# Kernel tuning notes

Measured on AMD Instinct MI355X. Metric: run time of the kernel, lower is better.

The kernel has to match this reference:

```python
import jax, jax.numpy as jnp
import numpy as np

V, E, H, L = 32000, 512, 1024, 2
B, S, T = 32, 64, 64


def setup_inputs() -> dict:
    key = jax.random.key(0)
    ks = jax.random.split(key, 16)
    sd = 0.05
    p = lambda k, shape: (jax.random.normal(k, shape, jnp.float32) * sd)
    z = lambda shape: jnp.zeros(shape, jnp.float32)
    return {
        "tgt_batch": jax.random.randint(ks[0], (B, S), 0, V),
        "enc_h": p(ks[1], (L, B, H)),
        "enc_c": p(ks[2], (L, B, H)),
        "enc_outputs": p(ks[3], (T, B, H)),
        "emb": p(ks[4], (V, E)),
        "W_ih0": p(ks[5], (4 * H, E + H)),
        "W_hh0": p(ks[6], (4 * H, H)),
        "b_ih0": z((4 * H,)),
        "b_hh0": z((4 * H,)),
        "W_ih1": p(ks[7], (4 * H, H)),
        "W_hh1": p(ks[8], (4 * H, H)),
        "b_ih1": z((4 * H,)),
        "b_hh1": z((4 * H,)),
        "Wa": p(ks[9], (H, 2 * H)),
        "ba": z((H,)),
        "va": p(ks[10], (H,)),
        "Wc": p(ks[11], (H, 2 * H)),
        "bc": z((H,)),
        "Wo": p(ks[12], (V, H)),
        "bo": z((V,)),
        "teacher_forcing": 1,
    }


def _lstm_cell(x, h, c, Wih, Whh, bih, bhh):
    # PyTorch gate order: i, f, g, o
    g = x @ Wih.T + bih + h @ Whh.T + bhh
    i, f, gg, o = jnp.split(g, 4, axis=1)
    c2 = jax.nn.sigmoid(f) * c + jax.nn.sigmoid(i) * jnp.tanh(gg)
    return jax.nn.sigmoid(o) * jnp.tanh(c2), c2


def reference(tgt_batch, enc_h, enc_c, enc_outputs, emb,
              W_ih0, W_hh0, b_ih0, b_hh0, W_ih1, W_hh1, b_ih1, b_hh1,
              Wa, ba, va, Wc, bc, Wo, bo, teacher_forcing):
    # teacher_forcing == 1 -> always feed the gold previous word (matches
    # the torch loop, whose sampling branch is never taken at tf=1.0).
    tgt = tgt_batch.T  # [S, B], seq-first

    def step(carry, x_t):
        h, c, attn_h = carry  # h,c: [L,B,H]; attn_h: [B,H]
        x = jnp.concatenate([emb[x_t], attn_h], axis=1)  # [B, E+H]
        h0, c0 = _lstm_cell(x, h[0], c[0], W_ih0, W_hh0, b_ih0, b_hh0)
        h1, c1 = _lstm_cell(h0, h[1], c[1], W_ih1, W_hh1, b_ih1, b_hh1)
        # additive ('concat') attention over encoder states, query = top h
        hid = jnp.broadcast_to(h1[None], enc_outputs.shape)  # [T,B,H]
        energy = jnp.tanh(jnp.concatenate([hid, enc_outputs], axis=-1) @ Wa.T + ba)
        scores = jnp.einsum('tbh,h->bt', energy, va)  # [B,T]
        weights = jax.nn.softmax(scores, axis=1)
        context = jnp.einsum('bt,tbh->bh', weights, enc_outputs)  # [B,H]
        attn_h2 = jnp.tanh(jnp.concatenate([h1, context], axis=1) @ Wc.T + bc)
        logp = jax.nn.log_softmax(attn_h2 @ Wo.T + bo, axis=1)  # [B,V]
        return (jnp.stack([h0, h1]), jnp.stack([c0, c1]), attn_h2), logp

    init = (enc_h, enc_c, jnp.zeros((tgt.shape[1], H), enc_h.dtype))
    _, dec_outputs = jax.lax.scan(step, init, tgt[:-1])  # [S-1, B, V]
    dec_output_words = jnp.argmax(dec_outputs, axis=-1).astype(jnp.int32)
    return dec_outputs, dec_output_words
```

## Files before the change

### kernel.cpp

```cpp
#include <hip/hip_runtime.h>
#include <math.h>

#define VOCAB 32000
#define EMBD  512
#define HID   1024
#define BATCH 32
#define SEQ   64
#define TENC  64
#define NSTEP 63
#define G4    4096

typedef __attribute__((ext_vector_type(8))) short short8;
typedef __attribute__((ext_vector_type(4))) float f32x4;
typedef __attribute__((ext_vector_type(4))) unsigned short us4;
typedef unsigned short u16;

__device__ __forceinline__ float4 ld4(const float* p) {
  return *reinterpret_cast<const float4*>(p);
}
__device__ __forceinline__ u16 f2bf(float x) {
  unsigned u = __float_as_uint(x);
  return (u16)((u + 0x7fffu + ((u >> 16) & 1u)) >> 16);
}
__device__ __forceinline__ float bf2f(u16 h) {
  return __uint_as_float(((unsigned)h) << 16);
}

template<int MODE>
__device__ __forceinline__ void mfma32(
    const u16* __restrict__ Xahi, const u16* __restrict__ Xalo,
    const u16* __restrict__ Xbhi, const u16* __restrict__ Xblo,
    const u16* __restrict__ Whi,  const u16* __restrict__ Wlo,
    int nt, float* res)
{
  const int tid = threadIdx.x;
  const int w = tid >> 6, l = tid & 63;
  const int c = l & 15, koct = l >> 4;
  constexpr int K   = (MODE == 0) ? 2048 : 1024;
  constexpr int WS  = (MODE == 0) ? 2048 : 1024;
  constexpr int SPW = K / 32 / 4;
  const int r0 = c, r1 = 16 + c;
  const int wr0 = (MODE == 0) ? ((r0 >> 3)*1024 + nt*8 + (r0 & 7)) : (nt*32 + r0);
  const int wr1 = (MODE == 0) ? ((r1 >> 3)*1024 + nt*8 + (r1 & 7)) : (nt*32 + r1);
  const u16* bh0 = Whi + (size_t)wr0 * WS;
  const u16* bh1 = Whi + (size_t)wr1 * WS;
  const u16* bl0 = Wlo + (size_t)wr0 * WS;
  const u16* bl1 = Wlo + (size_t)wr1 * WS;

  auto ldA = [&](int m, int kg, int lo) -> short8 {
    const u16* base;
    if (MODE == 0 && kg >= 1024) base = lo ? Xblo : Xbhi;
    else                         base = lo ? Xalo : Xahi;
    const int b = m*16 + c;
    return *reinterpret_cast<const short8*>(base + b*1024 + (kg & 1023));
  };

  f32x4 acc[2][2];
  #pragma unroll
  for (int m = 0; m < 2; ++m)
    #pragma unroll
    for (int n = 0; n < 2; ++n) acc[m][n] = (f32x4){0.f,0.f,0.f,0.f};

  const int s0 = w * SPW;
  short8 Ah[2], Al[2], Bh[2], Bl[2];
  {
    const int kg = s0*32 + koct*8;
    Ah[0]=ldA(0,kg,0); Ah[1]=ldA(1,kg,0); Al[0]=ldA(0,kg,1); Al[1]=ldA(1,kg,1);
    Bh[0]=*reinterpret_cast<const short8*>(bh0+kg);
    Bh[1]=*reinterpret_cast<const short8*>(bh1+kg);
    Bl[0]=*reinterpret_cast<const short8*>(bl0+kg);
    Bl[1]=*reinterpret_cast<const short8*>(bl1+kg);
  }
  for (int s = s0; s < s0 + SPW; ++s) {
    short8 nAh[2], nAl[2], nBh[2], nBl[2];
    if (s + 1 < s0 + SPW) {
      const int kg = (s+1)*32 + koct*8;
      nAh[0]=ldA(0,kg,0); nAh[1]=ldA(1,kg,0); nAl[0]=ldA(0,kg,1); nAl[1]=ldA(1,kg,1);
      nBh[0]=*reinterpret_cast<const short8*>(bh0+kg);
      nBh[1]=*reinterpret_cast<const short8*>(bh1+kg);
      nBl[0]=*reinterpret_cast<const short8*>(bl0+kg);
      nBl[1]=*reinterpret_cast<const short8*>(bl1+kg);
    }
    #pragma unroll
    for (int n = 0; n < 2; ++n)
      #pragma unroll
      for (int m = 0; m < 2; ++m) {
        acc[m][n] = __builtin_amdgcn_mfma_f32_16x16x32_bf16(Ah[m], Bh[n], acc[m][n], 0, 0, 0);
        acc[m][n] = __builtin_amdgcn_mfma_f32_16x16x32_bf16(Ah[m], Bl[n], acc[m][n], 0, 0, 0);
        acc[m][n] = __builtin_amdgcn_mfma_f32_16x16x32_bf16(Al[m], Bh[n], acc[m][n], 0, 0, 0);
      }
    #pragma unroll
    for (int i = 0; i < 2; ++i) { Ah[i]=nAh[i]; Al[i]=nAl[i]; Bh[i]=nBh[i]; Bl[i]=nBl[i]; }
  }
  #pragma unroll
  for (int m = 0; m < 2; ++m)
    #pragma unroll
    for (int n = 0; n < 2; ++n)
      #pragma unroll
      for (int r = 0; r < 4; ++r) {
        const int b = m*16 + koct*4 + r;
        const int rr = n*16 + c;
        res[w*1056 + b*33 + rr] = acc[m][n][r];
      }
}

struct GKM {
  const u16 *Xahi, *Xalo, *Xbhi, *Xblo;
  const u16 *Whi, *Wlo;
  const float* bsum; const float* gembt;
  float* c; u16 *hhi; u16 *hlo;
};

template<int HASGEMB>
__global__ __launch_bounds__(256) void gates_mfma_k(GKM P) {
  __shared__ float res[4*1056];
  mfma32<0>(P.Xahi, P.Xalo, P.Xbhi, P.Xblo, P.Whi, P.Wlo, blockIdx.x, res);
  __syncthreads();
  const int tid = threadIdx.x;
  const int b = tid >> 3, j = tid & 7;
  const int n = blockIdx.x*8 + j;
  float g4[4];
  #pragma unroll
  for (int g = 0; g < 4; ++g) {
    const int r = g*8 + j;
    float s = P.bsum[g*1024 + n]
            + res[b*33+r] + res[1056 + b*33+r] + res[2112 + b*33+r] + res[3168 + b*33+r];
    if (HASGEMB) s += P.gembt[(size_t)b*G4 + g*1024 + n];
    g4[g] = s;
  }
  const float si = 1.f/(1.f+expf(-g4[0]));
  const float sf = 1.f/(1.f+expf(-g4[1]));
  const float so = 1.f/(1.f+expf(-g4[3]));
  const int i = b*HID + n;
  const float cn = sf*P.c[i] + si*tanhf(g4[2]);
  P.c[i] = cn;
  const float h = so*tanhf(cn);
  const u16 hh = f2bf(h);
  P.hhi[i] = hh;
  P.hlo[i] = f2bf(h - bf2f(hh));
}

struct PKM {
  const u16 *Xhi, *Xlo; const u16 *Whi, *Wlo; float* Pq;
};

__global__ __launch_bounds__(256) void proj_mfma_k(PKM P) {
  __shared__ float res[4*1056];
  mfma32<1>(P.Xhi, P.Xlo, nullptr, nullptr, P.Whi, P.Wlo, blockIdx.x, res);
  __syncthreads();
  const int tid = threadIdx.x;
  #pragma unroll
  for (int q = 0; q < 4; ++q) {
    const int o = q*256 + tid;
    const int b = o >> 5, r = o & 31;
    const float s = res[b*33+r] + res[1056 + b*33+r]
                  + res[2112 + b*33+r] + res[3168 + b*33+r];
    P.Pq[(size_t)b*2048 + blockIdx.x*32 + r] = s;
  }
}

struct AKM {
  const float* Pq; const float* PreAC; const float* va; const float* bc;
  u16* AHthi; u16* AHtlo;
};

__global__ __launch_bounds__(1024) void attn_k(AKM P) {
  __shared__ float QS[HID];
  __shared__ float sw[TENC];
  __shared__ float W64[TENC];
  const int b = blockIdx.x;
  const int tid = threadIdx.x;
  QS[tid] = P.Pq[(size_t)b*2048 + tid];
  __syncthreads();
  const int lane = tid & 63, wid = tid >> 6;
  float vreg[16];
  #pragma unroll
  for (int i2 = 0; i2 < 16; ++i2) vreg[i2] = P.va[lane + 64*i2];
  #pragma unroll
  for (int j = 0; j < 4; ++j) {
    const int te = wid*4 + j;
    const float* pr = P.PreAC + ((size_t)te*BATCH + b)*2048;
    float s = 0.f;
    #pragma unroll
    for (int i2 = 0; i2 < 16; ++i2) {
      const int idx = lane + 64*i2;
      s += vreg[i2] * tanhf(QS[idx] + pr[idx]);
    }
    #pragma unroll
    for (int off = 32; off; off >>= 1) s += __shfl_xor(s, off);
    if (lane == 0) sw[te] = s;
  }
  __syncthreads();
  if (tid < TENC) {
    const float v = sw[tid];
    float mx = v;
    #pragma unroll
    for (int off = 32; off; off >>= 1) mx = fmaxf(mx, __shfl_xor(mx, off));
    const float e = expf(v - mx);
    float sum = e;
    #pragma unroll
    for (int off = 32; off; off >>= 1) sum += __shfl_xor(sum, off);
    W64[tid] = e / sum;
  }
  __syncthreads();
  const int hh = tid;
  float acc = 0.f;
  #pragma unroll 8
  for (int te = 0; te < TENC; ++te)
    acc += W64[te] * P.PreAC[((size_t)te*BATCH + b)*2048 + HID + hh];
  const float hc = P.Pq[(size_t)b*2048 + HID + hh] + P.bc[hh];
  const float ah = tanhf(acc + hc);
  const u16 ahh = f2bf(ah);
  P.AHthi[(size_t)b*HID + hh] = ahh;
  P.AHtlo[(size_t)b*HID + hh] = f2bf(ah - bf2f(ahh));
}

template<int MODE>
__global__ __launch_bounds__(256) void pack_k(const float* __restrict__ A,
                                              const float* __restrict__ B,
                                              u16* __restrict__ hi, u16* __restrict__ lo) {
  constexpr int ROWS = (MODE == 2) ? 2048 : 4096;
  constexpr int K    = (MODE == 2) ? 1024 : 2048;
  const size_t total = (size_t)ROWS * (K/4);
  for (size_t i = (size_t)blockIdx.x*256 + threadIdx.x; i < total;
       i += (size_t)gridDim.x*256) {
    const int row = (int)(i / (K/4));
    const int k = (int)(i % (K/4)) * 4;
    float4 v;
    if (MODE == 0) v = (k < 1024) ? ld4(A + (size_t)row*1536 + 512 + k)
                                  : ld4(B + (size_t)row*1024 + (k - 1024));
    else if (MODE == 1) v = (k < 1024) ? ld4(A + (size_t)row*1024 + k)
                                       : ld4(B + (size_t)row*1024 + (k - 1024));
    else v = (row < 1024) ? ld4(A + (size_t)row*2048 + k)
                          : ld4(B + (size_t)(row - 1024)*2048 + k);
    us4 h, l;
    h.x = f2bf(v.x); l.x = f2bf(v.x - bf2f(h.x));
    h.y = f2bf(v.y); l.y = f2bf(v.y - bf2f(h.y));
    h.z = f2bf(v.z); l.z = f2bf(v.z - bf2f(h.z));
    h.w = f2bf(v.w); l.w = f2bf(v.w - bf2f(h.w));
    *reinterpret_cast<us4*>(hi + i*4) = h;
    *reinterpret_cast<us4*>(lo + i*4) = l;
  }
}

__global__ __launch_bounds__(256) void cvt_k(const float* __restrict__ src,
                                             u16* __restrict__ hi,
                                             u16* __restrict__ lo, int n) {
  int i = (blockIdx.x*256 + threadIdx.x) * 4;
  const int stride = gridDim.x * 256 * 4;
  for (; i < n; i += stride) {
    const float4 v = ld4(src + i);
    us4 h, l;
    h.x = f2bf(v.x); l.x = f2bf(v.x - bf2f(h.x));
    h.y = f2bf(v.y); l.y = f2bf(v.y - bf2f(h.y));
    h.z = f2bf(v.z); l.z = f2bf(v.z - bf2f(h.z));
    h.w = f2bf(v.w); l.w = f2bf(v.w - bf2f(h.w));
    *reinterpret_cast<us4*>(hi + i) = h;
    *reinterpret_cast<us4*>(lo + i) = l;
  }
}

struct WGP {
  const float* A; const float* W; const float* W2; const float* bias;
  const int* tgt; const float* emb;
  float* C; int ldc;
};

template<int WM>
__device__ __forceinline__ float4 ldWL(const WGP& P, int r, int k) {
  if (WM == 2) return ld4(P.W + (size_t)r * (EMBD + HID) + k);
  if (r < HID) return ld4(P.W  + (size_t)r * (2*HID) + HID + k);
  return ld4(P.W2 + (size_t)(r - HID) * (2*HID) + HID + k);
}

template<int WM>
__device__ __forceinline__ float4 ldAL(const WGP& P, int row, int k) {
  if (WM == 2) {
    const int tok = P.tgt[(row & 31) * SEQ + (row >> 5)];
    return ld4(P.emb + (size_t)tok * EMBD + k);
  }
  return ld4(P.A + (size_t)row * 1024 + k);
}

template<int WM>
__global__ __launch_bounds__(256, 2) void gemmL(WGP P) {
  constexpr int KK = (WM == 2) ? 512 : 1024;
  __shared__ float At[32*36];
  __shared__ float Wt[32*260];
  const int tid = threadIdx.x;
  const int m0 = blockIdx.x * 32;
  const int n0 = blockIdx.y * 256;
  const int lr = tid >> 3, lc = (tid & 7) << 2;
  const int tn = tid & 31, tm = tid >> 5;
  float acc[4][8];
  #pragma unroll
  for (int i = 0; i < 4; ++i)
    #pragma unroll
    for (int x = 0; x < 8; ++x) acc[i][x] = 0.f;

  float4 av = ldAL<WM>(P, m0 + lr, lc);
  float4 wv[8];
  #pragma unroll
  for (int it = 0; it < 8; ++it) wv[it] = ldWL<WM>(P, n0 + lr + it*32, lc);

  for (int k0 = 0; k0 < KK; k0 += 32) {
    float4 avn, wvn[8];
    if (k0 + 32 < KK) {
      avn = ldAL<WM>(P, m0 + lr, k0 + 32 + lc);
      #pragma unroll
      for (int it = 0; it < 8; ++it) wvn[it] = ldWL<WM>(P, n0 + lr + it*32, k0 + 32 + lc);
    }
    __syncthreads();
    At[(lc+0)*36+lr]=av.x; At[(lc+1)*36+lr]=av.y; At[(lc+2)*36+lr]=av.z; At[(lc+3)*36+lr]=av.w;
    #pragma unroll
    for (int it = 0; it < 8; ++it) {
      const int r = lr + it*32;
      Wt[(lc+0)*260+r]=wv[it].x; Wt[(lc+1)*260+r]=wv[it].y;
      Wt[(lc+2)*260+r]=wv[it].z; Wt[(lc+3)*260+r]=wv[it].w;
    }
    __syncthreads();
    #pragma unroll
    for (int kk = 0; kk < 32; ++kk) {
      const float4 a  = *reinterpret_cast<const float4*>(&At[kk*36 + tm*4]);
      const float4 w0 = *reinterpret_cast<const float4*>(&Wt[kk*260 + tn*8]);
      const float4 w1 = *reinterpret_cast<const float4*>(&Wt[kk*260 + tn*8 + 4]);
      #pragma unroll
      for (int i = 0; i < 4; ++i) {
        const float ai = (&a.x)[i];
        acc[i][0]+=ai*w0.x; acc[i][1]+=ai*w0.y; acc[i][2]+=ai*w0.z; acc[i][3]+=ai*w0.w;
        acc[i][4]+=ai*w1.x; acc[i][5]+=ai*w1.y; acc[i][6]+=ai*w1.z; acc[i][7]+=ai*w1.w;
      }
    }
    av = avn;
    #pragma unroll
    for (int it = 0; it < 8; ++it) wv[it] = wvn[it];
  }
  const int na = n0 + tn*8, ma = m0 + tm*4;
  float bb[8];
  #pragma unroll
  for (int x = 0; x < 8; ++x) {
    if (WM == 1) bb[x] = (na + x < HID) ? P.bias[na+x] : 0.f;
    else         bb[x] = 0.f;
  }
  #pragma unroll
  for (int i = 0; i < 4; ++i)
    #pragma unroll
    for (int x = 0; x < 8; ++x)
      P.C[(size_t)(ma+i)*P.ldc + na + x] = acc[i][x] + bb[x];
}

struct LM {
  const u16* Ahi; const u16* Alo;
  const u16* Bhi; const u16* Blo;
  const float* bo; float* out;
};

__global__ __launch_bounds__(256) void logits_mfma(LM P) {
  __shared__ u16 sA[2][4][64][8];
  __shared__ u16 sB[2][4][128][8];
  const int tid = threadIdx.x;
  const int m0 = blockIdx.x * 64;
  const int n0 = blockIdx.y * 128;
  const int w = tid >> 6, l = tid & 63;
  const int mb = (w & 1) * 32, nb = (w >> 1) * 64;
  f32x4 acc[2][4];
  #pragma unroll
  for (int mt = 0; mt < 2; ++mt)
    #pragma unroll
    for (int nt = 0; nt < 4; ++nt) acc[mt][nt] = (f32x4){0.f,0.f,0.f,0.f};

  const int arow = tid >> 2, akg = tid & 3;
  const int brow = tid >> 1, bkg = (tid & 1) * 2;
  short8 pah, pal, pbh0, pbh1, pbl0, pbl1;
  {
    const size_t ao = (size_t)(m0 + arow)*HID + akg*8;
    const size_t bo0 = (size_t)(n0 + brow)*HID + bkg*8;
    pah  = *reinterpret_cast<const short8*>(P.Ahi + ao);
    pal  = *reinterpret_cast<const short8*>(P.Alo + ao);
    pbh0 = *reinterpret_cast<const short8*>(P.Bhi + bo0);
    pbh1 = *reinterpret_cast<const short8*>(P.Bhi + bo0 + 8);
    pbl0 = *reinterpret_cast<const short8*>(P.Blo + bo0);
    pbl1 = *reinterpret_cast<const short8*>(P.Blo + bo0 + 8);
  }
  for (int kc = 0; kc < 32; ++kc) {
    __syncthreads();
    *reinterpret_cast<short8*>(&sA[0][akg][arow][0]) = pah;
    *reinterpret_cast<short8*>(&sA[1][akg][arow][0]) = pal;
    *reinterpret_cast<short8*>(&sB[0][bkg  ][brow][0]) = pbh0;
    *reinterpret_cast<short8*>(&sB[0][bkg+1][brow][0]) = pbh1;
    *reinterpret_cast<short8*>(&sB[1][bkg  ][brow][0]) = pbl0;
    *reinterpret_cast<short8*>(&sB[1][bkg+1][brow][0]) = pbl1;
    __syncthreads();
    if (kc + 1 < 32) {
      const size_t ao = (size_t)(m0 + arow)*HID + (kc+1)*32 + akg*8;
      const size_t bo0 = (size_t)(n0 + brow)*HID + (kc+1)*32 + bkg*8;
      pah  = *reinterpret_cast<const short8*>(P.Ahi + ao);
      pal  = *reinterpret_cast<const short8*>(P.Alo + ao);
      pbh0 = *reinterpret_cast<const short8*>(P.Bhi + bo0);
      pbh1 = *reinterpret_cast<const short8*>(P.Bhi + bo0 + 8);
      pbl0 = *reinterpret_cast<const short8*>(P.Blo + bo0);
      pbl1 = *reinterpret_cast<const short8*>(P.Blo + bo0 + 8);
    }
    const int kg = l >> 4, rr = l & 15;
    short8 ah[2], al[2];
    #pragma unroll
    for (int mt = 0; mt < 2; ++mt) {
      ah[mt] = *reinterpret_cast<const short8*>(&sA[0][kg][mb + mt*16 + rr][0]);
      al[mt] = *reinterpret_cast<const short8*>(&sA[1][kg][mb + mt*16 + rr][0]);
    }
    #pragma unroll
    for (int nt = 0; nt < 4; ++nt) {
      const short8 bh = *reinterpret_cast<const short8*>(&sB[0][kg][nb + nt*16 + rr][0]);
      const short8 bl = *reinterpret_cast<const short8*>(&sB[1][kg][nb + nt*16 + rr][0]);
      #pragma unroll
      for (int mt = 0; mt < 2; ++mt) {
        acc[mt][nt] = __builtin_amdgcn_mfma_f32_16x16x32_bf16(ah[mt], bh, acc[mt][nt], 0, 0, 0);
        acc[mt][nt] = __builtin_amdgcn_mfma_f32_16x16x32_bf16(ah[mt], bl, acc[mt][nt], 0, 0, 0);
        acc[mt][nt] = __builtin_amdgcn_mfma_f32_16x16x32_bf16(al[mt], bh, acc[mt][nt], 0, 0, 0);
      }
    }
  }
  #pragma unroll
  for (int mt = 0; mt < 2; ++mt) {
    #pragma unroll
    for (int nt = 0; nt < 4; ++nt) {
      #pragma unroll
      for (int r = 0; r < 4; ++r) {
        const int row = m0 + mb + mt*16 + (l >> 4)*4 + r;
        const int col = n0 + nb + nt*16 + (l & 15);
        if (row < NSTEP*BATCH)
          P.out[(size_t)row*VOCAB + col] = acc[mt][nt][r] + P.bo[col];
      }
    }
  }
}

__global__ __launch_bounds__(256) void lsm_k(float* __restrict__ out,
                                             float* __restrict__ words) {
  const int b = blockIdx.x;
  const int t = blockIdx.y;
  float* row = out + ((size_t)t*BATCH + b)*VOCAB;
  const int tid = threadIdx.x;
  float m = -INFINITY; int mi = 0;
  for (int v = tid; v < VOCAB; v += 256) {
    const float x = row[v];
    if (x > m) { m = x; mi = v; }
  }
  __shared__ float sm[256]; __shared__ int si[256];
  sm[tid] = m; si[tid] = mi;
  __syncthreads();
  for (int s2 = 128; s2; s2 >>= 1) {
    if (tid < s2) {
      const float om = sm[tid+s2]; const int oi = si[tid+s2];
      if (om > sm[tid] || (om == sm[tid] && oi < si[tid])) { sm[tid]=om; si[tid]=oi; }
    }
    __syncthreads();
  }
  const float mx = sm[0]; const int amax = si[0];
  float s = 0.f;
  for (int v = tid; v < VOCAB; v += 256) s += expf(row[v]-mx);
  __shared__ float ss[256];
  ss[tid] = s; __syncthreads();
  for (int s2=128; s2; s2>>=1) { if (tid < s2) ss[tid] += ss[tid+s2]; __syncthreads(); }
  const float lse = logf(ss[0]) + mx;
  for (int v = tid; v < VOCAB; v += 256) row[v] = row[v] - lse;
  if (tid == 0) words[(size_t)t*BATCH + b] = (float)amax;
}

__global__ __launch_bounds__(256) void init_k(const float* __restrict__ enc_h,
                                              const float* __restrict__ enc_c,
                                              const float* __restrict__ bih0,
                                              const float* __restrict__ bhh0,
                                              const float* __restrict__ bih1,
                                              const float* __restrict__ bhh1,
                                              float* c0, float* c1,
                                              u16* h0hi, u16* h0lo, u16* h1hi, u16* h1lo,
                                              u16* zahhi, u16* zahlo,
                                              float* bsum0, float* bsum1) {
  const int i = blockIdx.x*256 + threadIdx.x;
  if (i < BATCH*HID) {
    c0[i] = enc_c[i]; c1[i] = enc_c[BATCH*HID + i];
    const float v0 = enc_h[i];
    const u16 h0 = f2bf(v0);
    h0hi[i] = h0; h0lo[i] = f2bf(v0 - bf2f(h0));
    const float v1 = enc_h[BATCH*HID + i];
    const u16 h1 = f2bf(v1);
    h1hi[i] = h1; h1lo[i] = f2bf(v1 - bf2f(h1));
    zahhi[i] = 0; zahlo[i] = 0;
  }
  if (i < G4) {
    bsum0[i] = bih0[i] + bhh0[i];
    bsum1[i] = bih1[i] + bhh1[i];
  }
}

extern "C" void kernel_launch(void* const* d_in, const int* in_sizes, int n_in,
                              void* d_out, int out_size, void* d_ws, size_t ws_size,
                              hipStream_t stream) {
  const int*   tgt   = (const int*)d_in[0];
  const float* enc_h = (const float*)d_in[1];
  const float* enc_c = (const float*)d_in[2];
  const float* enc   = (const float*)d_in[3];
  const float* emb   = (const float*)d_in[4];
  const float* Wih0  = (const float*)d_in[5];
  const float* Whh0  = (const float*)d_in[6];
  const float* bih0  = (const float*)d_in[7];
  const float* bhh0  = (const float*)d_in[8];
  const float* Wih1  = (const float*)d_in[9];
  const float* Whh1  = (const float*)d_in[10];
  const float* bih1  = (const float*)d_in[11];
  const float* bhh1  = (const float*)d_in[12];
  const float* Wa    = (const float*)d_in[13];
  const float* ba    = (const float*)d_in[14];
  const float* va    = (const float*)d_in[15];
  const float* Wc    = (const float*)d_in[16];
  const float* bc    = (const float*)d_in[17];
  const float* Wo    = (const float*)d_in[18];
  const float* bo    = (const float*)d_in[19];

  u16* AHhi = (u16*)d_ws;
  u16* AHlo = AHhi + (size_t)2048*1024;
  float* pool = (float*)(AHlo + (size_t)2048*1024);

  float* PreAC = pool;
  float* Gemb  = PreAC + (size_t)2048*2048;
  float* Pq    = Gemb  + (size_t)NSTEP*BATCH*G4;
  float* c0    = Pq    + (size_t)BATCH*2048;
  float* c1v   = c0    + BATCH*HID;
  float* bsum0 = c1v   + BATCH*HID;
  float* bsum1 = bsum0 + G4;
  u16* W0hi = (u16*)(bsum1 + G4);
  u16* W0lo = W0hi + (size_t)4096*2048;
  u16* W1hi = W0lo + (size_t)4096*2048;
  u16* W1lo = W1hi + (size_t)4096*2048;
  u16* WAhi = W1lo + (size_t)4096*2048;
  u16* WAlo = WAhi + (size_t)2048*1024;
  u16* h0Ahi = WAlo + (size_t)2048*1024;
  u16* h0Alo = h0Ahi + BATCH*HID;
  u16* h0Bhi = h0Alo + BATCH*HID;
  u16* h0Blo = h0Bhi + BATCH*HID;
  u16* h1Ahi = h0Blo + BATCH*HID;
  u16* h1Alo = h1Ahi + BATCH*HID;
  u16* h1Bhi = h1Alo + BATCH*HID;
  u16* h1Blo = h1Bhi + BATCH*HID;
  u16* zahhi = h1Blo + BATCH*HID;
  u16* zahlo = zahhi + BATCH*HID;
  u16* Wohi = (u16*)pool;
  u16* Wolo = Wohi + (size_t)VOCAB*1024;

  float* out   = (float*)d_out;
  float* words = out + (size_t)NSTEP*BATCH*VOCAB;

  init_k<<<dim3(128), 256, 0, stream>>>(enc_h, enc_c, bih0, bhh0, bih1, bhh1,
                                        c0, c1v, h0Ahi, h0Alo, h1Ahi, h1Alo,
                                        zahhi, zahlo, bsum0, bsum1);

  {
    WGP p = {}; p.A = enc; p.W = Wa; p.W2 = Wc; p.bias = ba; p.C = PreAC; p.ldc = 2048;
    gemmL<1><<<dim3(64, 8), 256, 0, stream>>>(p);
  }
  {
    WGP p = {}; p.W = Wih0; p.tgt = tgt; p.emb = emb; p.C = Gemb; p.ldc = G4;
    gemmL<2><<<dim3(NSTEP*BATCH/32, G4/256), 256, 0, stream>>>(p);
  }
  pack_k<0><<<dim3(1024), 256, 0, stream>>>(Wih0, Whh0, W0hi, W0lo);
  pack_k<1><<<dim3(1024), 256, 0, stream>>>(Wih1, Whh1, W1hi, W1lo);
  pack_k<2><<<dim3(512), 256, 0, stream>>>(Wa, Wc, WAhi, WAlo);

  for (int t = 0; t < NSTEP; ++t) {
    const u16* ahphi = t ? (AHhi + (size_t)(t-1)*BATCH*HID) : zahhi;
    const u16* ahplo = t ? (AHlo + (size_t)(t-1)*BATCH*HID) : zahlo;
    const u16* h0phi = (t & 1) ? h0Bhi : h0Ahi;
    const u16* h0plo = (t & 1) ? h0Blo : h0Alo;
    u16* h0chi = (t & 1) ? h0Ahi : h0Bhi;
    u16* h0clo = (t & 1) ? h0Alo : h0Blo;
    const u16* h1phi = (t & 1) ? h1Bhi : h1Ahi;
    const u16* h1plo = (t & 1) ? h1Blo : h1Alo;
    u16* h1chi = (t & 1) ? h1Ahi : h1Bhi;
    u16* h1clo = (t & 1) ? h1Alo : h1Blo;

    {
      GKM p = {};
      p.Xahi = ahphi; p.Xalo = ahplo; p.Xbhi = h0phi; p.Xblo = h0plo;
      p.Whi = W0hi; p.Wlo = W0lo;
      p.bsum = bsum0; p.gembt = Gemb + (size_t)t*BATCH*G4;
      p.c = c0; p.hhi = h0chi; p.hlo = h0clo;
      gates_mfma_k<1><<<dim3(128), 256, 0, stream>>>(p);
    }
    {
      GKM p = {};
      p.Xahi = h0chi; p.Xalo = h0clo; p.Xbhi = h1phi; p.Xblo = h1plo;
      p.Whi = W1hi; p.Wlo = W1lo;
      p.bsum = bsum1; p.gembt = nullptr;
      p.c = c1v; p.hhi = h1chi; p.hlo = h1clo;
      gates_mfma_k<0><<<dim3(128), 256, 0, stream>>>(p);
    }
    {
      PKM p; p.Xhi = h1chi; p.Xlo = h1clo; p.Whi = WAhi; p.Wlo = WAlo; p.Pq = Pq;
      proj_mfma_k<<<dim3(64), 256, 0, stream>>>(p);
    }
    {
      AKM p; p.Pq = Pq; p.PreAC = PreAC; p.va = va; p.bc = bc;
      p.AHthi = AHhi + (size_t)t*BATCH*HID;
      p.AHtlo = AHlo + (size_t)t*BATCH*HID;
      attn_k<<<dim3(BATCH), 1024, 0, stream>>>(p);
    }
  }

  cvt_k<<<dim3(4096), 256, 0, stream>>>(Wo, Wohi, Wolo, VOCAB*1024);
  {
    LM p; p.Ahi = AHhi; p.Alo = AHlo; p.Bhi = Wohi; p.Blo = Wolo;
    p.bo = bo; p.out = out;
    logits_mfma<<<dim3(32, VOCAB/128), 256, 0, stream>>>(p);
  }
  lsm_k<<<dim3(BATCH, NSTEP), 256, 0, stream>>>(out, words);
}
```

Baseline: 5.914 ms.

## Move encoder and embedding precompute GEMMs to split-bf16 MFMA tile kernel

Adds a generic split-bf16 MFMA tile kernel, with an optional token-gather on the A operand, and uses it for the encoder attention projection and the embedding input-gate precompute. These previously ran through the older gemmL path. Inputs are first converted to hi/lo bf16 pairs in extra workspace, with a fallback to the old path when the workspace is too small. The logits GEMM now uses the same kernel with a 1D grid. Log-softmax switches to an online max/sum in one pass with 512 threads.

New measurement: 6.062 ms. +2.5%, slower.

```diff
diff --git a/kernel.cpp b/kernel.cpp
--- a/kernel.cpp
+++ b/kernel.cpp
@@ -215,12 +215,114 @@
   P.AHtlo[(size_t)b*HID + hh] = f2bf(ah - bf2f(ahh));
 }
 
+struct TM {
+  const u16 *Ahi, *Alo, *Bhi, *Blo;
+  const int* tgt; const float* bias;
+  float* out; int ldc, M, ntile_n;
+};
+
+template<int NC, int AMODE>
+__global__ __launch_bounds__(256) void tile_k(TM P) {
+  __shared__ float smemf[6144];
+  u16* sA = (u16*)smemf;
+  u16* sB = sA + 4096;
+  constexpr int K = NC * 32;
+  const int tile = blockIdx.x;
+  const int mi = tile / P.ntile_n, ni = tile % P.ntile_n;
+  const int m0 = mi * 64, n0 = ni * 128;
+  const int tid = threadIdx.x;
+  const int w = tid >> 6, l = tid & 63;
+  const int mb = (w & 1) * 32, nb = (w >> 1) * 64;
+  f32x4 acc[2][4];
+  #pragma unroll
+  for (int mt = 0; mt < 2; ++mt)
+    #pragma unroll
+    for (int nt = 0; nt < 4; ++nt) acc[mt][nt] = (f32x4){0.f,0.f,0.f,0.f};
+
+  const int arow = tid >> 2, akg = tid & 3;
+  const int brow = tid >> 1, bkg = (tid & 1) * 2;
+  size_t arbase;
+  if (AMODE == 1) {
+    const int row = m0 + arow;
+    const int tok = P.tgt[(row & 31)*SEQ + (row >> 5)];
+    arbase = (size_t)tok * K;
+  } else {
+    arbase = (size_t)(m0 + arow) * K;
+  }
+  const size_t brbase = (size_t)(n0 + brow) * K;
+
+  short8 pah, pal, pbh0, pbh1, pbl0, pbl1;
+  {
+    const size_t ao = arbase + akg*8;
+    const size_t bo0 = brbase + bkg*8;
+    pah  = *reinterpret_cast<const short8*>(P.Ahi + ao);
+    pal  = *reinterpret_cast<const short8*>(P.Alo + ao);
+    pbh0 = *reinterpret_cast<const short8*>(P.Bhi + bo0);
+    pbh1 = *reinterpret_cast<const short8*>(P.Bhi + bo0 + 8);
+    pbl0 = *reinterpret_cast<const short8*>(P.Blo + bo0);
+    pbl1 = *reinterpret_cast<const short8*>(P.Blo + bo0 + 8);
+  }
+  for (int kc = 0; kc < NC; ++kc) {
+    __syncthreads();
+    *reinterpret_cast<short8*>(sA + ((0*4 + akg)*64 + arow)*8) = pah;
+    *reinterpret_cast<short8*>(sA + ((1*4 + akg)*64 + arow)*8) = pal;
+    *reinterpret_cast<short8*>(sB + ((0*4 + bkg  )*128 + brow)*8) = pbh0;
+    *reinterpret_cast<short8*>(sB + ((0*4 + bkg+1)*128 + brow)*8) = pbh1;
+    *reinterpret_cast<short8*>(sB + ((1*4 + bkg  )*128 + brow)*8) = pbl0;
+    *reinterpret_cast<short8*>(sB + ((1*4 + bkg+1)*128 + brow)*8) = pbl1;
+    __syncthreads();
+    if (kc + 1 < NC) {
+      const size_t ao = arbase + (kc+1)*32 + akg*8;
+      const size_t bo0 = brbase + (kc+1)*32 + bkg*8;
+      pah  = *reinterpret_cast<const short8*>(P.Ahi + ao);
+      pal  = *reinterpret_cast<const short8*>(P.Alo + ao);
+      pbh0 = *reinterpret_cast<const short8*>(P.Bhi + bo0);
+      pbh1 = *reinterpret_cast<const short8*>(P.Bhi + bo0 + 8);
+      pbl0 = *reinterpret_cast<const short8*>(P.Blo + bo0);
+      pbl1 = *reinterpret_cast<const short8*>(P.Blo + bo0 + 8);
+    }
+    const int kg = l >> 4, rr = l & 15;
+    short8 ah[2], al[2];
+    #pragma unroll
+    for (int mt = 0; mt < 2; ++mt) {
+      ah[mt] = *reinterpret_cast<const short8*>(sA + ((0*4 + kg)*64 + mb + mt*16 + rr)*8);
+      al[mt] = *reinterpret_cast<const short8*>(sA + ((1*4 + kg)*64 + mb + mt*16 + rr)*8);
+    }
+    #pragma unroll
+    for (int nt = 0; nt < 4; ++nt) {
+      const short8 bh = *reinterpret_cast<const short8*>(sB + ((0*4 + kg)*128 + nb + nt*16 + rr)*8);
+      const short8 bl = *reinterpret_cast<const short8*>(sB + ((1*4 + kg)*128 + nb + nt*16 + rr)*8);
+      #pragma unroll
+      for (int mt = 0; mt < 2; ++mt) {
+        acc[mt][nt] = __builtin_amdgcn_mfma_f32_16x16x32_bf16(ah[mt], bh, acc[mt][nt], 0, 0, 0);
+        acc[mt][nt] = __builtin_amdgcn_mfma_f32_16x16x32_bf16(ah[mt], bl, acc[mt][nt], 0, 0, 0);
+        acc[mt][nt] = __builtin_amdgcn_mfma_f32_16x16x32_bf16(al[mt], bh, acc[mt][nt], 0, 0, 0);
+      }
+    }
+  }
+  #pragma unroll
+  for (int mt = 0; mt < 2; ++mt) {
+    #pragma unroll
+    for (int nt = 0; nt < 4; ++nt) {
+      #pragma unroll
+      for (int r = 0; r < 4; ++r) {
+        const int row = m0 + mb + mt*16 + (l >> 4)*4 + r;
+        const int col = n0 + nb + nt*16 + (l & 15);
+        if (row < P.M) {
+          const float bb = P.bias ? P.bias[col] : 0.f;
+          P.out[(size_t)row*P.ldc + col] = acc[mt][nt][r] + bb;
+        }
+      }
+    }
+  }
+}
+
 template<int MODE>
 __global__ __launch_bounds__(256) void pack_k(const float* __restrict__ A,
                                               const float* __restrict__ B,
                                               u16* __restrict__ hi, u16* __restrict__ lo) {
-  constexpr int ROWS = (MODE == 2) ? 2048 : 4096;
-  constexpr int K    = (MODE == 2) ? 1024 : 2048;
+  constexpr int ROWS = (MODE == 2 || MODE == 3) ? 2048 : 4096;
+  constexpr int K    = (MODE == 2 || MODE == 3) ? 1024 : (MODE == 4 ? 512 : 2048);
   const size_t total = (size_t)ROWS * (K/4);
   for (size_t i = (size_t)blockIdx.x*256 + threadIdx.x; i < total;
        i += (size_t)gridDim.x*256) {
@@ -231,8 +333,11 @@
                                   : ld4(B + (size_t)row*1024 + (k - 1024));
     else if (MODE == 1) v = (k < 1024) ? ld4(A + (size_t)row*1024 + k)
                                        : ld4(B + (size_t)row*1024 + (k - 1024));
-    else v = (row < 1024) ? ld4(A + (size_t)row*2048 + k)
-                          : ld4(B + (size_t)(row - 1024)*2048 + k);
+    else if (MODE == 2) v = (row < 1024) ? ld4(A + (size_t)row*2048 + k)
+                                         : ld4(B + (size_t)(row - 1024)*2048 + k);
+    else if (MODE == 3) v = (row < 1024) ? ld4(A + (size_t)row*2048 + 1024 + k)
+                                         : ld4(B + (size_t)(row - 1024)*2048 + 1024 + k);
+    else v = ld4(A + (size_t)row*1536 + k);
     us4 h, l;
     h.x = f2bf(v.x); l.x = f2bf(v.x - bf2f(h.x));
     h.y = f2bf(v.y); l.y = f2bf(v.y - bf2f(h.y));
@@ -349,121 +454,39 @@
       P.C[(size_t)(ma+i)*P.ldc + na + x] = acc[i][x] + bb[x];
 }
 
-struct LM {
-  const u16* Ahi; const u16* Alo;
-  const u16* Bhi; const u16* Blo;
-  const float* bo; float* out;
-};
-
-__global__ __launch_bounds__(256) void logits_mfma(LM P) {
-  __shared__ u16 sA[2][4][64][8];
-  __shared__ u16 sB[2][4][128][8];
-  const int tid = threadIdx.x;
-  const int m0 = blockIdx.x * 64;
-  const int n0 = blockIdx.y * 128;
-  const int w = tid >> 6, l = tid & 63;
-  const int mb = (w & 1) * 32, nb = (w >> 1) * 64;
-  f32x4 acc[2][4];
-  #pragma unroll
-  for (int mt = 0; mt < 2; ++mt)
-    #pragma unroll
-    for (int nt = 0; nt < 4; ++nt) acc[mt][nt] = (f32x4){0.f,0.f,0.f,0.f};
-
-  const int arow = tid >> 2, akg = tid & 3;
-  const int brow = tid >> 1, bkg = (tid & 1) * 2;
-  short8 pah, pal, pbh0, pbh1, pbl0, pbl1;
-  {
-    const size_t ao = (size_t)(m0 + arow)*HID + akg*8;
-    const size_t bo0 = (size_t)(n0 + brow)*HID + bkg*8;
-    pah  = *reinterpret_cast<const short8*>(P.Ahi + ao);
-    pal  = *reinterpret_cast<const short8*>(P.Alo + ao);
-    pbh0 = *reinterpret_cast<const short8*>(P.Bhi + bo0);
-    pbh1 = *reinterpret_cast<const short8*>(P.Bhi + bo0 + 8);
-    pbl0 = *reinterpret_cast<const short8*>(P.Blo + bo0);
-    pbl1 = *reinterpret_cast<const short8*>(P.Blo + bo0 + 8);
-  }
-  for (int kc = 0; kc < 32; ++kc) {
-    __syncthreads();
-    *reinterpret_cast<short8*>(&sA[0][akg][arow][0]) = pah;
-    *reinterpret_cast<short8*>(&sA[1][akg][arow][0]) = pal;
-    *reinterpret_cast<short8*>(&sB[0][bkg  ][brow][0]) = pbh0;
-    *reinterpret_cast<short8*>(&sB[0][bkg+1][brow][0]) = pbh1;
-    *reinterpret_cast<short8*>(&sB[1][bkg  ][brow][0]) = pbl0;
-    *reinterpret_cast<short8*>(&sB[1][bkg+1][brow][0]) = pbl1;
-    __syncthreads();
-    if (kc + 1 < 32) {
-      const size_t ao = (size_t)(m0 + arow)*HID + (kc+1)*32 + akg*8;
-      const size_t bo0 = (size_t)(n0 + brow)*HID + (kc+1)*32 + bkg*8;
-      pah  = *reinterpret_cast<const short8*>(P.Ahi + ao);
-      pal  = *reinterpret_cast<const short8*>(P.Alo + ao);
-      pbh0 = *reinterpret_cast<const short8*>(P.Bhi + bo0);
-      pbh1 = *reinterpret_cast<const short8*>(P.Bhi + bo0 + 8);
-      pbl0 = *reinterpret_cast<const short8*>(P.Blo + bo0);
-      pbl1 = *reinterpret_cast<const short8*>(P.Blo + bo0 + 8);
-    }
-    const int kg = l >> 4, rr = l & 15;
-    short8 ah[2], al[2];
-    #pragma unroll
-    for (int mt = 0; mt < 2; ++mt) {
-      ah[mt] = *reinterpret_cast<const short8*>(&sA[0][kg][mb + mt*16 + rr][0]);
-      al[mt] = *reinterpret_cast<const short8*>(&sA[1][kg][mb + mt*16 + rr][0]);
-    }
-    #pragma unroll
-    for (int nt = 0; nt < 4; ++nt) {
-      const short8 bh = *reinterpret_cast<const short8*>(&sB[0][kg][nb + nt*16 + rr][0]);
-      const short8 bl = *reinterpret_cast<const short8*>(&sB[1][kg][nb + nt*16 + rr][0]);
-      #pragma unroll
-      for (int mt = 0; mt < 2; ++mt) {
-        acc[mt][nt] = __builtin_amdgcn_mfma_f32_16x16x32_bf16(ah[mt], bh, acc[mt][nt], 0, 0, 0);
-        acc[mt][nt] = __builtin_amdgcn_mfma_f32_16x16x32_bf16(ah[mt], bl, acc[mt][nt], 0, 0, 0);
-        acc[mt][nt] = __builtin_amdgcn_mfma_f32_16x16x32_bf16(al[mt], bh, acc[mt][nt], 0, 0, 0);
-      }
-    }
-  }
-  #pragma unroll
-  for (int mt = 0; mt < 2; ++mt) {
-    #pragma unroll
-    for (int nt = 0; nt < 4; ++nt) {
-      #pragma unroll
-      for (int r = 0; r < 4; ++r) {
-        const int row = m0 + mb + mt*16 + (l >> 4)*4 + r;
-        const int col = n0 + nb + nt*16 + (l & 15);
-        if (row < NSTEP*BATCH)
-          P.out[(size_t)row*VOCAB + col] = acc[mt][nt][r] + P.bo[col];
-      }
-    }
-  }
-}
-
-__global__ __launch_bounds__(256) void lsm_k(float* __restrict__ out,
+__global__ __launch_bounds__(512) void lsm_k(float* __restrict__ out,
                                              float* __restrict__ words) {
   const int b = blockIdx.x;
   const int t = blockIdx.y;
   float* row = out + ((size_t)t*BATCH + b)*VOCAB;
   const int tid = threadIdx.x;
-  float m = -INFINITY; int mi = 0;
-  for (int v = tid; v < VOCAB; v += 256) {
+  float m = -INFINITY, s = 0.f; int mi = 0;
+  for (int v = tid; v < VOCAB; v += 512) {
     const float x = row[v];
-    if (x > m) { m = x; mi = v; }
-  }
-  __shared__ float sm[256]; __shared__ int si[256];
-  sm[tid] = m; si[tid] = mi;
+    if (x > m) { s = s * expf(m - x) + 1.f; m = x; mi = v; }
+    else s += expf(x - m);
+  }
+  __shared__ float sm[512]; __shared__ float sv[512]; __shared__ int si[512];
+  sm[tid] = m; sv[tid] = s; si[tid] = mi;
   __syncthreads();
-  for (int s2 = 128; s2; s2 >>= 1) {
-    if (tid < s2) {
-      const float om = sm[tid+s2]; const int oi = si[tid+s2];
-      if (om > sm[tid] || (om == sm[tid] && oi < si[tid])) { sm[tid]=om; si[tid]=oi; }
+  for (int st = 256; st; st >>= 1) {
+    if (tid < st) {
+      const float om = sm[tid+st], os = sv[tid+st]; const int oi = si[tid+st];
+      if (om > sm[tid]) {
+        sv[tid] = os + sv[tid] * expf(sm[tid] - om);
+        sm[tid] = om; si[tid] = oi;
+      } else if (om == sm[tid]) {
+        sv[tid] += os;
+        if (oi < si[tid]) si[tid] = oi;
+      } else {
+        sv[tid] += os * expf(om - sm[tid]);
+      }
     }
     __syncthreads();
   }
-  const float mx = sm[0]; const int amax = si[0];
-  float s = 0.f;
-  for (int v = tid; v < VOCAB; v += 256) s += expf(row[v]-mx);
-  __shared__ float ss[256];
-  ss[tid] = s; __syncthreads();
-  for (int s2=128; s2; s2>>=1) { if (tid < s2) ss[tid] += ss[tid+s2]; __syncthreads(); }
-  const float lse = logf(ss[0]) + mx;
-  for (int v = tid; v < VOCAB; v += 256) row[v] = row[v] - lse;
+  const float lse = logf(sv[0]) + sm[0];
+  const int amax = si[0];
+  for (int v = tid; v < VOCAB; v += 512) row[v] = row[v] - lse;
   if (tid == 0) words[(size_t)t*BATCH + b] = (float)amax;
 }
 
@@ -473,10 +496,12 @@
                                               const float* __restrict__ bhh0,
                                               const float* __restrict__ bih1,
                                               const float* __restrict__ bhh1,
+                                              const float* __restrict__ ba,
                                               float* c0, float* c1,
                                               u16* h0hi, u16* h0lo, u16* h1hi, u16* h1lo,
                                               u16* zahhi, u16* zahlo,
-                                              float* bsum0, float* bsum1) {
+                                              float* bsum0, float* bsum1,
+                                              float* bias2048) {
   const int i = blockIdx.x*256 + threadIdx.x;
   if (i < BATCH*HID) {
     c0[i] = enc_c[i]; c1[i] = enc_c[BATCH*HID + i];
@@ -492,6 +517,7 @@
     bsum0[i] = bih0[i] + bhh0[i];
     bsum1[i] = bih1[i] + bhh1[i];
   }
+  if (i < 2048) bias2048[i] = (i < HID) ? ba[i] : 0.f;
 }
 
 extern "C" void kernel_launch(void* const* d_in, const int* in_sizes, int n_in,
@@ -518,50 +544,79 @@
   const float* Wo    = (const float*)d_in[18];
   const float* bo    = (const float*)d_in[19];
 
-  u16* AHhi = (u16*)d_ws;
-  u16* AHlo = AHhi + (size_t)2048*1024;
-  float* pool = (float*)(AHlo + (size_t)2048*1024);
-
-  float* PreAC = pool;
-  float* Gemb  = PreAC + (size_t)2048*2048;
-  float* Pq    = Gemb  + (size_t)NSTEP*BATCH*G4;
-  float* c0    = Pq    + (size_t)BATCH*2048;
-  float* c1v   = c0    + BATCH*HID;
-  float* bsum0 = c1v   + BATCH*HID;
-  float* bsum1 = bsum0 + G4;
-  u16* W0hi = (u16*)(bsum1 + G4);
-  u16* W0lo = W0hi + (size_t)4096*2048;
-  u16* W1hi = W0lo + (size_t)4096*2048;
-  u16* W1lo = W1hi + (size_t)4096*2048;
-  u16* WAhi = W1lo + (size_t)4096*2048;
-  u16* WAlo = WAhi + (size_t)2048*1024;
-  u16* h0Ahi = WAlo + (size_t)2048*1024;
-  u16* h0Alo = h0Ahi + BATCH*HID;
-  u16* h0Bhi = h0Alo + BATCH*HID;
-  u16* h0Blo = h0Bhi + BATCH*HID;
-  u16* h1Ahi = h0Blo + BATCH*HID;
-  u16* h1Alo = h1Ahi + BATCH*HID;
-  u16* h1Bhi = h1Alo + BATCH*HID;
-  u16* h1Blo = h1Bhi + BATCH*HID;
-  u16* zahhi = h1Blo + BATCH*HID;
-  u16* zahlo = zahhi + BATCH*HID;
-  u16* Wohi = (u16*)pool;
+  char* base = (char*)d_ws;
+  size_t cur = 0;
+  auto take = [&](size_t bytes) { char* p = base + cur; cur = (cur + bytes + 63) & ~(size_t)63; return p; };
+
+  u16* AHhi = (u16*)take((size_t)2048*1024*2);
+  u16* AHlo = (u16*)take((size_t)2048*1024*2);
+  float* PreAC = (float*)take((size_t)2048*2048*4);
+  float* Gemb  = (float*)take((size_t)NSTEP*BATCH*G4*4);
+  float* Pq    = (float*)take((size_t)BATCH*2048*4);
+  float* c0    = (float*)take(BATCH*HID*4);
+  float* c1v   = (float*)take(BATCH*HID*4);
+  float* bsum0 = (float*)take(G4*4);
+  float* bsum1 = (float*)take(G4*4);
+  float* bias2048 = (float*)take(2048*4);
+  u16* W0hi = (u16*)take((size_t)4096*2048*2);
+  u16* W0lo = (u16*)take((size_t)4096*2048*2);
+  u16* W1hi = (u16*)take((size_t)4096*2048*2);
+  u16* W1lo = (u16*)take((size_t)4096*2048*2);
+  u16* WAhi = (u16*)take((size_t)2048*1024*2);
+  u16* WAlo = (u16*)take((size_t)2048*1024*2);
+  u16* h0Ahi = (u16*)take(BATCH*HID*2);
+  u16* h0Alo = (u16*)take(BATCH*HID*2);
+  u16* h0Bhi = (u16*)take(BATCH*HID*2);
+  u16* h0Blo = (u16*)take(BATCH*HID*2);
+  u16* h1Ahi = (u16*)take(BATCH*HID*2);
+  u16* h1Alo = (u16*)take(BATCH*HID*2);
+  u16* h1Bhi = (u16*)take(BATCH*HID*2);
+  u16* h1Blo = (u16*)take(BATCH*HID*2);
+  u16* zahhi = (u16*)take(BATCH*HID*2);
+  u16* zahlo = (u16*)take(BATCH*HID*2);
+  char* S = take((size_t)VOCAB*1024*2*2);
+  const bool fast = ws_size >= cur;
+
+  u16* enchi = (u16*)S;
+  u16* enclo = enchi + (size_t)2048*1024;
+  u16* embhi = enclo + (size_t)2048*1024;
+  u16* emblo = embhi + (size_t)VOCAB*EMBD;
+  u16* WAChi = emblo + (size_t)VOCAB*EMBD;
+  u16* WAClo = WAChi + (size_t)2048*1024;
+  u16* W0ehi = WAClo + (size_t)2048*1024;
+  u16* W0elo = W0ehi + (size_t)4096*512;
+  u16* Wohi = fast ? (u16*)S : (u16*)PreAC;
   u16* Wolo = Wohi + (size_t)VOCAB*1024;
 
   float* out   = (float*)d_out;
   float* words = out + (size_t)NSTEP*BATCH*VOCAB;
 
-  init_k<<<dim3(128), 256, 0, stream>>>(enc_h, enc_c, bih0, bhh0, bih1, bhh1,
+  init_k<<<dim3(128), 256, 0, stream>>>(enc_h, enc_c, bih0, bhh0, bih1, bhh1, ba,
                                         c0, c1v, h0Ahi, h0Alo, h1Ahi, h1Alo,
-                                        zahhi, zahlo, bsum0, bsum1);
-
-  {
-    WGP p = {}; p.A = enc; p.W = Wa; p.W2 = Wc; p.bias = ba; p.C = PreAC; p.ldc = 2048;
-    gemmL<1><<<dim3(64, 8), 256, 0, stream>>>(p);
-  }
-  {
-    WGP p = {}; p.W = Wih0; p.tgt = tgt; p.emb = emb; p.C = Gemb; p.ldc = G4;
-    gemmL<2><<<dim3(NSTEP*BATCH/32, G4/256), 256, 0, stream>>>(p);
+                                        zahhi, zahlo, bsum0, bsum1, bias2048);
+
+  if (fast) {
+    cvt_k<<<dim3(512), 256, 0, stream>>>(enc, enchi, enclo, 2048*1024);
+    cvt_k<<<dim3(4096), 256, 0, stream>>>(emb, embhi, emblo, VOCAB*EMBD);
+    pack_k<3><<<dim3(512), 256, 0, stream>>>(Wa, Wc, WAChi, WAClo);
+    pack_k<4><<<dim3(512), 256, 0, stream>>>(Wih0, nullptr, W0ehi, W0elo);
+    {
+      TM p; p.Ahi = enchi; p.Alo = enclo; p.Bhi = WAChi; p.Blo = WAClo;
+      p.tgt = nullptr; p.bias = bias2048; p.out = PreAC;
+      p.ldc = 2048; p.M = 2048; p.ntile_n = 16;
+      tile_k<32,0><<<dim3(512), 256, 0, stream>>>(p);
+    }
+    {
+      TM p; p.Ahi = embhi; p.Alo = emblo; p.Bhi = W0ehi; p.Blo = W0elo;
+      p.tgt = tgt; p.bias = nullptr; p.out = Gemb;
+      p.ldc = G4; p.M = NSTEP*BATCH; p.ntile_n = 32;
+      tile_k<16,1><<<dim3(1024), 256, 0, stream>>>(p);
+    }
+  } else {
+    { WGP p = {}; p.A = enc; p.W = Wa; p.W2 = Wc; p.bias = ba; p.C = PreAC; p.ldc = 2048;
+      gemmL<1><<<dim3(64, 8), 256, 0, stream>>>(p); }
+    { WGP p = {}; p.W = Wih0; p.tgt = tgt; p.emb = emb; p.C = Gemb; p.ldc = G4;
+      gemmL<2><<<dim3(NSTEP*BATCH/32, G4/256), 256, 0, stream>>>(p); }
   }
   pack_k<0><<<dim3(1024), 256, 0, stream>>>(Wih0, Whh0, W0hi, W0lo);
   pack_k<1><<<dim3(1024), 256, 0, stream>>>(Wih1, Whh1, W1hi, W1lo);
@@ -609,9 +664,10 @@
 
   cvt_k<<<dim3(4096), 256, 0, stream>>>(Wo, Wohi, Wolo, VOCAB*1024);
   {
-    LM p; p.Ahi = AHhi; p.Alo = AHlo; p.Bhi = Wohi; p.Blo = Wolo;
-    p.bo = bo; p.out = out;
-    logits_mfma<<<dim3(32, VOCAB/128), 256, 0, stream>>>(p);
-  }
-  lsm_k<<<dim3(BATCH, NSTEP), 256, 0, stream>>>(out, words);
-}
+    TM p; p.Ahi = AHhi; p.Alo = AHlo; p.Bhi = Wohi; p.Blo = Wolo;
+    p.tgt = nullptr; p.bias = bo; p.out = out;
+    p.ldc = VOCAB; p.M = NSTEP*BATCH; p.ntile_n = 250;
+    tile_k<32,0><<<dim3(8000), 256, 0, stream>>>(p);
+  }
+  lsm_k<<<dim3(BATCH, NSTEP), 512, 0, stream>>>(out, words);
+}
```
